# Optimization experiments

Measured on AMD Instinct MI355X. Metric: run time of the kernel, lower is better.

The kernel has to match this reference:

```python
import jax, jax.numpy as jnp
import numpy as np

DIM = 1024

def setup_inputs() -> dict:
    key = jax.random.key(0)
    k1, k2, k3, k4, k5 = jax.random.split(key, 5)
    B, Sq, Skv = 8, 2048, 2048
    x = jax.random.normal(k1, (B, Sq, DIM), dtype=jnp.float32)
    context = jax.random.normal(k2, (B, Skv, DIM), dtype=jnp.float32)
    # nn.Linear default init scale ~ uniform; use scaled normal for stability
    s = DIM ** -0.5
    Wq = jax.random.normal(k3, (DIM, DIM), dtype=jnp.float32) * s
    Wk = jax.random.normal(k4, (DIM, DIM), dtype=jnp.float32) * s
    Wv = jax.random.normal(k5, (DIM, DIM), dtype=jnp.float32) * s
    return {"x": x, "context": context, "Wq": Wq, "Wk": Wk, "Wv": Wv}

def reference(x, context, Wq, Wk, Wv):
    # Linear with weight W applied as x @ W.T (torch convention); here W is [out, in]
    q = jnp.einsum('bsd,ed->bse', x, Wq)          # [B, Sq, D]
    k = jnp.einsum('btd,ed->bte', context, Wk)    # [B, Skv, D]
    v = jnp.einsum('btd,ed->bte', context, Wv)    # [B, Skv, D]
    scale = Wq.shape[0] ** -0.5                   # dim ** -0.5 (no head split)
    dots = jnp.einsum('bse,bte->bst', q, k) * scale  # [B, Sq, Skv]
    attn = jax.nn.softmax(dots, axis=-1)
    out = jnp.einsum('bst,bte->bse', attn, v)     # [B, Sq, D]
    return out
```

## Files before the change

kernel.cpp:

```cpp
#include <hip/hip_runtime.h>


typedef unsigned short u16;
typedef __bf16 bf16x8 __attribute__((ext_vector_type(8)));
typedef float f32x4 __attribute__((ext_vector_type(4)));
typedef u16 us8 __attribute__((ext_vector_type(8)));

__device__ __forceinline__ u16 f2bf(float f) {
  unsigned int u = __float_as_uint(f);
  u += 0x7fffu + ((u >> 16) & 1u);
  return (u16)(u >> 16);
}
__device__ __forceinline__ float bf2f(u16 h) {
  return __uint_as_float((unsigned int)h << 16);
}

struct __attribute__((aligned(8))) us4 { u16 x, y, z, w; };

__global__ __launch_bounds__(256) void cvt_xc(const float4* __restrict__ x,
                                              const float4* __restrict__ c,
                                              us4* __restrict__ dx,
                                              us4* __restrict__ dc) {
  int i = blockIdx.x * 256 + threadIdx.x;
  const float4* s = (i < 4194304) ? x : (c - 4194304);
  us4* d = (i < 4194304) ? dx : (dc - 4194304);
  float4 v = s[i];
  us4 o{f2bf(v.x), f2bf(v.y), f2bf(v.z), f2bf(v.w)};
  d[i] = o;
}

__global__ __launch_bounds__(256) void cvt_w(const float4* __restrict__ wq,
                                             const float4* __restrict__ wk,
                                             const float4* __restrict__ wv,
                                             us4* __restrict__ d) {
  int i = blockIdx.x * 256 + threadIdx.x;
  const float4* s; float sc;
  if (i < 262144)      { s = wq;           sc = 0.03125f; }
  else if (i < 524288) { s = wk - 262144;  sc = 1.0f; }
  else                 { s = wv - 524288;  sc = 1.0f; }
  float4 v = s[i];
  us4 o{f2bf(v.x * sc), f2bf(v.y * sc), f2bf(v.z * sc), f2bf(v.w * sc)};
  d[i] = o;
}

__device__ __forceinline__ void gload16(const u16* g, u16* l) {
  __builtin_amdgcn_global_load_lds(
      (const __attribute__((address_space(1))) unsigned int*)g,
      (__attribute__((address_space(3))) unsigned int*)l,
      16, 0, 0);
}

template <bool BF16OUT>
__global__ __launch_bounds__(512) void gemm_nt(
    const u16* __restrict__ A, const u16* __restrict__ B, void* __restrict__ Cout,
    int lda, int ldb, int ldc, int K,
    long batchA, long batchB, long batchC, int nx, int ny) {
  __shared__ u16 sA[256 * 32];
  __shared__ u16 sB[128 * 32];

  const int p    = blockIdx.x;
  const int slab = gridDim.x >> 3;
  const int gid  = (p & 7) * slab + (p >> 3);
  const int bx   = gid % nx;
  const int t2   = gid / nx;
  const int by   = t2 % ny;
  const int z    = t2 / ny;

  const int tid  = threadIdx.x;
  const int lane = tid & 63;
  const int wv   = tid >> 6;

  const u16* Ab = A + (size_t)z * batchA + (size_t)by * 256 * lda;
  const u16* Bb = B + (size_t)z * batchB + (size_t)bx * 128 * ldb;

  const int srow = tid >> 2;
  const int scol = (tid & 3) * 8;

  const u16* gA0 = Ab + (size_t)srow * lda + scol;
  const u16* gA1 = Ab + (size_t)(128 + srow) * lda + scol;
  const u16* gB  = Bb + (size_t)srow * ldb + scol;

  const int fr = lane & 15;
  const int fq = (lane >> 4) * 8;
  const int wm = (wv & 3) * 64;
  const int wn = (wv >> 2) * 64;

  f32x4 acc[4][4];
#pragma unroll
  for (int i = 0; i < 4; i++)
#pragma unroll
    for (int j = 0; j < 4; j++) acc[i][j] = (f32x4)0.f;

  for (int k0 = 0; k0 < K; k0 += 32) {
    gload16(gA0 + k0, &sA[tid * 8]);
    gload16(gA1 + k0, &sA[4096 + tid * 8]);
    gload16(gB  + k0, &sB[tid * 8]);
    __syncthreads();

    bf16x8 av[4], bv[4];
#pragma unroll
    for (int i = 0; i < 4; i++)
      av[i] = *(const bf16x8*)&sA[(wm + i * 16 + fr) * 32 + fq];
#pragma unroll
    for (int i = 0; i < 4; i++)
      bv[i] = *(const bf16x8*)&sB[(wn + i * 16 + fr) * 32 + fq];
#pragma unroll
    for (int mi = 0; mi < 4; mi++)
#pragma unroll
      for (int ni = 0; ni < 4; ni++)
        acc[mi][ni] = __builtin_amdgcn_mfma_f32_16x16x32_bf16(
            av[mi], bv[ni], acc[mi][ni], 0, 0, 0);
    __syncthreads();
  }

  const size_t cbase = (size_t)z * batchC;
  const int row0 = by * 256 + wm + (lane >> 4) * 4;
  const int col0 = bx * 128 + wn + fr;
#pragma unroll
  for (int mi = 0; mi < 4; mi++) {
#pragma unroll
    for (int i = 0; i < 4; i++) {
      const size_t roff = cbase + (size_t)(row0 + mi * 16 + i) * ldc + col0;
#pragma unroll
      for (int ni = 0; ni < 4; ni++) {
        float v = acc[mi][ni][i];
        if constexpr (BF16OUT)
          ((u16*)Cout)[roff + ni * 16] = f2bf(v);
        else
          ((float*)Cout)[roff + ni * 16] = v;
      }
    }
  }
}

__global__ __launch_bounds__(256) void softmax_rows_bf16(u16* __restrict__ SP) {
  const size_t row = blockIdx.x;
  us8* p = (us8*)(SP + row * 2048);
  const int t = threadIdx.x;
  us8 raw = p[t];
  float v[8];
#pragma unroll
  for (int i = 0; i < 8; i++) v[i] = bf2f(raw[i]);

  float m = v[0];
#pragma unroll
  for (int i = 1; i < 8; i++) m = fmaxf(m, v[i]);
#pragma unroll
  for (int o = 32; o; o >>= 1) m = fmaxf(m, __shfl_xor(m, o, 64));
  __shared__ float redm[4];
  if ((t & 63) == 0) redm[t >> 6] = m;
  __syncthreads();
  m = fmaxf(fmaxf(redm[0], redm[1]), fmaxf(redm[2], redm[3]));

  float sum = 0.f;
#pragma unroll
  for (int i = 0; i < 8; i++) { v[i] = __expf(v[i] - m); sum += v[i]; }
#pragma unroll
  for (int o = 32; o; o >>= 1) sum += __shfl_xor(sum, o, 64);
  __shared__ float reds[4];
  if ((t & 63) == 0) reds[t >> 6] = sum;
  __syncthreads();
  sum = reds[0] + reds[1] + reds[2] + reds[3];
  const float r = 1.0f / sum;

  us8 o;
#pragma unroll
  for (int i = 0; i < 8; i++) o[i] = f2bf(v[i] * r);
  p[t] = o;
}

extern "C" void kernel_launch(void* const* d_in, const int* in_sizes, int n_in,
                              void* d_out, int out_size, void* d_ws, size_t ws_size,
                              hipStream_t stream) {
  const float* x   = (const float*)d_in[0];
  const float* ctx = (const float*)d_in[1];
  const float* Wq  = (const float*)d_in[2];
  const float* Wk  = (const float*)d_in[3];
  const float* Wv  = (const float*)d_in[4];
  float* out = (float*)d_out;

  const size_t NT = 8ull * 2048 * 1024;

  u16* wsu  = (u16*)d_ws;
  u16* xbf  = wsu;
  u16* cbf  = wsu + NT;
  u16* Sbuf = wsu;
  u16* Vt   = wsu + 2 * NT;
  u16* Wqb  = wsu + 3 * NT;
  u16* Qbf = (u16*)d_out;

  dim3 blk(256), gblk(512);

  cvt_xc<<<dim3(32768), blk, 0, stream>>>((const float4*)x, (const float4*)ctx,
                                          (us4*)xbf, (us4*)cbf);
  cvt_w<<<dim3(3072), blk, 0, stream>>>((const float4*)Wq, (const float4*)Wk,
                                        (const float4*)Wv, (us4*)Wqb);

  gemm_nt<true><<<dim3(1024), gblk, 0, stream>>>(
      xbf, Wqb, Qbf, 1024, 1024, 1024, 1024,
      (long)NT, 1024L * 1024, (long)NT, 8, 64);
  gemm_nt<true><<<dim3(512), gblk, 0, stream>>>(
      Wqb + 2 * 1024 * 1024, cbf, Vt, 1024, 1024, 2048, 1024,
      0L, 2048L * 1024, 1024L * 2048, 16, 4);

  gemm_nt<true><<<dim3(1024), gblk, 0, stream>>>(
      Qbf, Qbf + NT, Sbuf, 1024, 1024, 2048, 1024,
      2048L * 1024, 2048L * 1024, 2048L * 2048, 16, 8);

  softmax_rows_bf16<<<dim3(16384), blk, 0, stream>>>(Sbuf);

  gemm_nt<false><<<dim3(512), gblk, 0, stream>>>(
      Sbuf, Vt, out, 2048, 2048, 1024, 2048,
      2048L * 2048, 1024L * 2048, 2048L * 1024, 8, 8);
}
```

Before: 453.6 us.

## Enlarge GEMM tile to 256x256 with double-buffered LDS prefetch and swizzle

The GEMM kernel now uses a 256x256 output tile with a K-step of 64, split into two 32-wide halves. It double-buffers shared memory so global-to-LDS loads for the next K tile overlap with MFMA work on the current one, using explicit vmcnt waits and barriers. An XOR swizzle on LDS columns is meant to cut bank conflicts, and s_setprio raises priority around MFMA blocks. Grid sizes are halved to match the larger tile. The trade-off is 128KB of LDS and a larger accumulator register footprint, which may limit occupancy.

```diff
diff --git a/kernel.cpp b/kernel.cpp
--- a/kernel.cpp
+++ b/kernel.cpp
@@ -51,12 +51,11 @@
 }
 
 template <bool BF16OUT>
-__global__ __launch_bounds__(512) void gemm_nt(
+__global__ __launch_bounds__(512, 2) void gemm_nt(
     const u16* __restrict__ A, const u16* __restrict__ B, void* __restrict__ Cout,
     int lda, int ldb, int ldc, int K,
     long batchA, long batchB, long batchC, int nx, int ny) {
-  __shared__ u16 sA[256 * 32];
-  __shared__ u16 sB[128 * 32];
+  __shared__ u16 lds[65536];
 
   const int p    = blockIdx.x;
   const int slab = gridDim.x >> 3;
@@ -71,53 +70,103 @@
   const int wv   = tid >> 6;
 
   const u16* Ab = A + (size_t)z * batchA + (size_t)by * 256 * lda;
-  const u16* Bb = B + (size_t)z * batchB + (size_t)bx * 128 * ldb;
+  const u16* Bb = B + (size_t)z * batchB + (size_t)bx * 256 * ldb;
 
   const int srow = tid >> 2;
-  const int scol = (tid & 3) * 8;
-
-  const u16* gA0 = Ab + (size_t)srow * lda + scol;
-  const u16* gA1 = Ab + (size_t)(128 + srow) * lda + scol;
-  const u16* gB  = Bb + (size_t)srow * ldb + scol;
+  const int scol = ((tid & 3) ^ ((tid >> 3) & 3)) * 8;
+
+  const u16* gA = Ab + (size_t)srow * lda + scol;
+  const u16* gB = Bb + (size_t)srow * ldb + scol;
+  const size_t a128 = (size_t)128 * lda, b128 = (size_t)128 * ldb;
+
+  u16* dA = &lds[tid * 8];
+  u16* dB = &lds[16384 + tid * 8];
 
   const int fr = lane & 15;
-  const int fq = (lane >> 4) * 8;
-  const int wm = (wv & 3) * 64;
-  const int wn = (wv >> 2) * 64;
-
-  f32x4 acc[4][4];
-#pragma unroll
-  for (int i = 0; i < 4; i++)
+  const int xw = (((lane >> 4) ^ ((lane >> 1) & 3)) * 8);
+  const int wm = (wv >> 2) * 128;
+  const int wn = (wv & 3) * 64;
+  const int rA = (wm + fr) * 32 + xw;
+  const int rB = (wn + fr) * 32 + xw;
+
+  f32x4 acc[8][4];
+#pragma unroll
+  for (int i = 0; i < 8; i++)
 #pragma unroll
     for (int j = 0; j < 4; j++) acc[i][j] = (f32x4)0.f;
 
-  for (int k0 = 0; k0 < K; k0 += 32) {
-    gload16(gA0 + k0, &sA[tid * 8]);
-    gload16(gA1 + k0, &sA[4096 + tid * 8]);
-    gload16(gB  + k0, &sB[tid * 8]);
-    __syncthreads();
-
+  const int NTt = K >> 6;
+
+#define STAGE_A(BUF, KT, H) do {                                  \
+    const u16* g_ = gA + (size_t)(KT) * 64 + (H) * 32;            \
+    u16* d_ = dA + ((BUF) << 15) + (H) * 8192;                    \
+    gload16(g_, d_); gload16(g_ + a128, d_ + 4096); } while (0)
+#define STAGE_B(BUF, KT, H) do {                                  \
+    const u16* g_ = gB + (size_t)(KT) * 64 + (H) * 32;            \
+    u16* d_ = dB + ((BUF) << 15) + (H) * 8192;                    \
+    gload16(g_, d_); gload16(g_ + b128, d_ + 4096); } while (0)
+#define LOAD_AV(H, ROFF) _Pragma("unroll")                        \
+    for (int i_ = 0; i_ < 4; i_++)                                \
+      av[i_] = *(const bf16x8*)&lds[cb + (H) * 8192 + rA + (ROFF) + i_ * 512];
+#define LOAD_BV(H) _Pragma("unroll")                              \
+    for (int i_ = 0; i_ < 4; i_++)                                \
+      bv[i_] = *(const bf16x8*)&lds[cb + 16384 + (H) * 8192 + rB + i_ * 512];
+#define MFMA16(AR)                                                \
+    __builtin_amdgcn_s_setprio(1);                                \
+    _Pragma("unroll")                                             \
+    for (int mi_ = 0; mi_ < 4; mi_++)                             \
+      _Pragma("unroll")                                           \
+      for (int ni_ = 0; ni_ < 4; ni_++)                           \
+        acc[(AR) + mi_][ni_] = __builtin_amdgcn_mfma_f32_16x16x32_bf16( \
+            av[mi_], bv[ni_], acc[(AR) + mi_][ni_], 0, 0, 0);     \
+    __builtin_amdgcn_s_setprio(0);
+
+  STAGE_A(0, 0, 0); STAGE_B(0, 0, 0); STAGE_A(0, 0, 1); STAGE_B(0, 0, 1);
+  asm volatile("s_waitcnt vmcnt(4)" ::: "memory");
+  __builtin_amdgcn_s_barrier();
+  __builtin_amdgcn_sched_barrier(0);
+
+  for (int kt = 0; kt < NTt; ++kt) {
+    const int cb = (kt & 1) << 15;
+    const int nb = (kt & 1) ^ 1;
+    const bool pf = (kt + 1 < NTt);
     bf16x8 av[4], bv[4];
-#pragma unroll
-    for (int i = 0; i < 4; i++)
-      av[i] = *(const bf16x8*)&sA[(wm + i * 16 + fr) * 32 + fq];
-#pragma unroll
-    for (int i = 0; i < 4; i++)
-      bv[i] = *(const bf16x8*)&sB[(wn + i * 16 + fr) * 32 + fq];
-#pragma unroll
-    for (int mi = 0; mi < 4; mi++)
-#pragma unroll
-      for (int ni = 0; ni < 4; ni++)
-        acc[mi][ni] = __builtin_amdgcn_mfma_f32_16x16x32_bf16(
-            av[mi], bv[ni], acc[mi][ni], 0, 0, 0);
-    __syncthreads();
+
+    if (pf) STAGE_A(nb, kt + 1, 0);
+    LOAD_AV(0, 0)
+    LOAD_BV(0)
+    MFMA16(0)
+
+    if (pf) STAGE_B(nb, kt + 1, 0);
+    LOAD_AV(0, 2048)
+    MFMA16(4)
+
+    if (pf) { asm volatile("s_waitcnt vmcnt(4)" ::: "memory"); }
+    else    { asm volatile("s_waitcnt vmcnt(0)" ::: "memory"); }
+    __builtin_amdgcn_s_barrier();
+    __builtin_amdgcn_sched_barrier(0);
+
+    if (pf) STAGE_A(nb, kt + 1, 1);
+    LOAD_AV(1, 0)
+    LOAD_BV(1)
+    MFMA16(0)
+
+    if (pf) STAGE_B(nb, kt + 1, 1);
+    LOAD_AV(1, 2048)
+    MFMA16(4)
+
+    if (pf) {
+      asm volatile("s_waitcnt vmcnt(4)" ::: "memory");
+      __builtin_amdgcn_s_barrier();
+      __builtin_amdgcn_sched_barrier(0);
+    }
   }
 
   const size_t cbase = (size_t)z * batchC;
   const int row0 = by * 256 + wm + (lane >> 4) * 4;
-  const int col0 = bx * 128 + wn + fr;
-#pragma unroll
-  for (int mi = 0; mi < 4; mi++) {
+  const int col0 = bx * 256 + wn + fr;
+#pragma unroll
+  for (int mi = 0; mi < 8; mi++) {
 #pragma unroll
     for (int i = 0; i < 4; i++) {
       const size_t roff = cbase + (size_t)(row0 + mi * 16 + i) * ldc + col0;
@@ -131,6 +180,11 @@
       }
     }
   }
+#undef STAGE_A
+#undef STAGE_B
+#undef LOAD_AV
+#undef LOAD_BV
+#undef MFMA16
 }
 
 __global__ __launch_bounds__(256) void softmax_rows_bf16(u16* __restrict__ SP) {
@@ -196,20 +250,20 @@
   cvt_w<<<dim3(3072), blk, 0, stream>>>((const float4*)Wq, (const float4*)Wk,
                                         (const float4*)Wv, (us4*)Wqb);
 
-  gemm_nt<true><<<dim3(1024), gblk, 0, stream>>>(
+  gemm_nt<true><<<dim3(512), gblk, 0, stream>>>(
       xbf, Wqb, Qbf, 1024, 1024, 1024, 1024,
-      (long)NT, 1024L * 1024, (long)NT, 8, 64);
+      (long)NT, 1024L * 1024, (long)NT, 4, 64);
+  gemm_nt<true><<<dim3(256), gblk, 0, stream>>>(
+      Wqb + 2 * 1024 * 1024, cbf, Vt, 1024, 1024, 2048, 1024,
+      0L, 2048L * 1024, 1024L * 2048, 8, 4);
+
   gemm_nt<true><<<dim3(512), gblk, 0, stream>>>(
-      Wqb + 2 * 1024 * 1024, cbf, Vt, 1024, 1024, 2048, 1024,
-      0L, 2048L * 1024, 1024L * 2048, 16, 4);
-
-  gemm_nt<true><<<dim3(1024), gblk, 0, stream>>>(
       Qbf, Qbf + NT, Sbuf, 1024, 1024, 2048, 1024,
-      2048L * 1024, 2048L * 1024, 2048L * 2048, 16, 8);
+      2048L * 1024, 2048L * 1024, 2048L * 2048, 8, 8);
 
   softmax_rows_bf16<<<dim3(16384), blk, 0, stream>>>(Sbuf);
 
-  gemm_nt<false><<<dim3(512), gblk, 0, stream>>>(
+  gemm_nt<false><<<dim3(256), gblk, 0, stream>>>(
       Sbuf, Vt, out, 2048, 2048, 1024, 2048,
-      2048L * 2048, 1024L * 2048, 2048L * 1024, 8, 8);
-}
+      2048L * 2048, 1024L * 2048, 2048L * 1024, 4, 8);
+}
```

After: 433.4 us. 4.5% less time.
